# Performance work log

Measured on AMD Instinct MI355X. Metric: run time of the kernel, lower is better.

Reference implementation:

```python
import jax, jax.numpy as jnp
import numpy as np

EPS = 1e-8  # matches F.cosine_similarity default eps


def setup_inputs() -> dict:
    key = jax.random.key(0)
    k1, k2 = jax.random.split(key)
    labels = jax.random.uniform(k1, (8192, 2), dtype=jnp.float32)  # argmax -> random 0/1
    datas = jax.random.normal(k2, (8192, 4096), dtype=jnp.float32)
    return {"labels": labels, "datas": datas}


def reference(labels, datas):
    # labels: [B, C] one-hot (C=2); datas: [B, D]
    lab = jnp.argmax(labels, axis=1)
    mask0 = (lab == 0).astype(datas.dtype)  # normal vectors
    mask1 = (lab == 1).astype(datas.dtype)  # except vectors
    n0 = jnp.sum(mask0)
    n1 = jnp.sum(mask1)

    # mean of label-0 rows (fixed-shape masked mean instead of boolean gather)
    mean_vec = jnp.sum(datas * mask0[:, None], axis=0) / jnp.maximum(n0, 1.0)  # [D]

    # batched cosine similarity of every row vs mean_vec (replaces per-row loop)
    x_norm = jnp.maximum(jnp.linalg.norm(datas, axis=1), EPS)  # [B]
    m_norm = jnp.maximum(jnp.linalg.norm(mean_vec), EPS)       # scalar
    cos = (datas @ mean_vec) / (x_norm * m_norm)               # [B]
    abs_cos = jnp.abs(cos)

    sim_loss = jnp.sum(mask0 * (1.0 - abs_cos)) / jnp.maximum(n0, 1.0)
    differ_loss = jnp.sum(mask1 * abs_cos) / jnp.maximum(n1, 1.0)

    # edge cases: no normals -> both 0; normals but no excepts -> differ 0
    sim_loss = jnp.where(n0 > 0, sim_loss, 0.0)
    differ_loss = jnp.where((n0 > 0) & (n1 > 0), differ_loss, 0.0)
    total_loss = sim_loss + differ_loss
    return (total_loss, sim_loss, differ_loss)
```

## Files before the change

kernel.cpp:

```cpp
#include <hip/hip_runtime.h>
#include <math.h>

#define NROWS 8192
#define NCOLS 4096
#define NC4 1024
#define EPS 1e-8f

__device__ float g_partials[256 * NCOLS];
__device__ float g_S[NCOLS];
__device__ float g_n0[256];
__device__ float g_msq[64];
__device__ float g_A[2048];
__device__ float g_B[2048];

__global__ __launch_bounds__(1024) void k_colsum(const float* __restrict__ labels,
                                                 const float* __restrict__ datas) {
    const int b = blockIdx.x, t = threadIdx.x;
    const int r0 = b * 32;
    __shared__ float shm[32];
    if (t < 32) {
        float l0 = labels[2 * (r0 + t)];
        float l1 = labels[2 * (r0 + t) + 1];
        shm[t] = (l0 >= l1) ? 1.f : 0.f;
    }
    __syncthreads();
    if (t == 0) {
        float c = 0.f;
        #pragma unroll
        for (int r = 0; r < 32; ++r) c += shm[r];
        g_n0[b] = c;
    }
    const float4* d4 = (const float4*)datas;
    float4 acc = {0.f, 0.f, 0.f, 0.f};
    for (int r = 0; r < 32; ++r) {
        if (shm[r] != 0.f) {
            float4 v = d4[(size_t)(r0 + r) * NC4 + t];
            acc.x += v.x; acc.y += v.y; acc.z += v.z; acc.w += v.w;
        }
    }
    ((float4*)g_partials)[(size_t)b * NC4 + t] = acc;
}

__global__ __launch_bounds__(1024) void k_reduceS() {
    const int t = threadIdx.x, b = blockIdx.x;
    const int col = t & 63, sub = t >> 6;
    const int c = b * 64 + col;
    float s = 0.f;
    #pragma unroll
    for (int j = 0; j < 16; ++j)
        s += g_partials[(size_t)(sub * 16 + j) * NCOLS + c];
    __shared__ float sh[16][65];
    sh[sub][col] = s;
    __syncthreads();
    if (t < 64) {
        float tot = 0.f;
        #pragma unroll
        for (int i = 0; i < 16; ++i) tot += sh[i][t];
        g_S[c] = tot;
        float sq = tot * tot;
        #pragma unroll
        for (int off = 32; off; off >>= 1) sq += __shfl_xor(sq, off);
        if (t == 0) g_msq[b] = sq;
    }
}

__global__ __launch_bounds__(256) void k_cos(const float* __restrict__ labels,
                                             const float* __restrict__ datas) {
    const int t = threadIdx.x, lane = t & 63, w = t >> 6;
    const int r = blockIdx.x * 4 + w;
    const float4* d4 = (const float4*)datas;
    const float4* s4 = (const float4*)g_S;
    const size_t base = (size_t)r * NC4;
    float dot = 0.f, sq = 0.f;
    float4 v[8];
    #pragma unroll
    for (int half = 0; half < 2; ++half) {
        #pragma unroll
        for (int k = 0; k < 8; ++k)
            v[k] = d4[base + lane + ((half * 8 + k) << 6)];
        #pragma unroll
        for (int k = 0; k < 8; ++k) {
            float4 sv = s4[lane + ((half * 8 + k) << 6)];
            dot += v[k].x * sv.x + v[k].y * sv.y + v[k].z * sv.z + v[k].w * sv.w;
            sq  += v[k].x * v[k].x + v[k].y * v[k].y + v[k].z * v[k].z + v[k].w * v[k].w;
        }
    }
    #pragma unroll
    for (int off = 32; off; off >>= 1) {
        dot += __shfl_xor(dot, off);
        sq  += __shfl_xor(sq, off);
    }
    __shared__ float shA[4], shB[4];
    if (lane == 0) {
        float a = fabsf(dot) / fmaxf(sqrtf(sq), EPS);
        float l0 = labels[2 * r], l1 = labels[2 * r + 1];
        bool m0 = (l0 >= l1);
        shA[w] = m0 ? a : 0.f;
        shB[w] = m0 ? 0.f : a;
    }
    __syncthreads();
    if (t == 0) {
        g_A[blockIdx.x] = shA[0] + shA[1] + shA[2] + shA[3];
        g_B[blockIdx.x] = shB[0] + shB[1] + shB[2] + shB[3];
    }
}

__global__ __launch_bounds__(1024) void k_final(float* __restrict__ out) {
    const int t = threadIdx.x, lane = t & 63, w = t >> 6;
    float A = g_A[t] + g_A[t + 1024];
    float B = g_B[t] + g_B[t + 1024];
    float n0 = (t < 256) ? g_n0[t] : 0.f;
    float msq = (t < 64) ? g_msq[t] : 0.f;
    #pragma unroll
    for (int off = 32; off; off >>= 1) {
        A   += __shfl_xor(A, off);
        B   += __shfl_xor(B, off);
        n0  += __shfl_xor(n0, off);
        msq += __shfl_xor(msq, off);
    }
    __shared__ float sh[16][4];
    if (lane == 0) { sh[w][0] = A; sh[w][1] = B; sh[w][2] = n0; sh[w][3] = msq; }
    __syncthreads();
    if (t == 0) {
        float At = 0.f, Bt = 0.f, n0t = 0.f, mt = 0.f;
        #pragma unroll
        for (int i = 0; i < 16; ++i) {
            At += sh[i][0]; Bt += sh[i][1]; n0t += sh[i][2]; mt += sh[i][3];
        }
        float n1 = (float)NROWS - n0t;
        float n0d = fmaxf(n0t, 1.f), n1d = fmaxf(n1, 1.f);
        float D = fmaxf(sqrtf(mt), n0d * EPS);
        float simL = (n0t > 0.f) ? (n0t - At / D) / n0d : 0.f;
        float difL = (n0t > 0.f && n1 > 0.f) ? (Bt / D) / n1d : 0.f;
        out[0] = simL + difL;
        out[1] = simL;
        out[2] = difL;
    }
}

extern "C" void kernel_launch(void* const* d_in, const int* in_sizes, int n_in,
                              void* d_out, int out_size, void* d_ws, size_t ws_size,
                              hipStream_t stream) {
    const float* labels = (const float*)d_in[0];
    const float* datas  = (const float*)d_in[1];
    float* out = (float*)d_out;

    k_colsum<<<256, 1024, 0, stream>>>(labels, datas);
    k_reduceS<<<64, 1024, 0, stream>>>();
    k_cos<<<2048, 256, 0, stream>>>(labels, datas);
    k_final<<<1, 1024, 0, stream>>>(out);
}
```

Measured before the change: 208.7 us.

## Compact masked rows, split colsum blocks, stage mean in LDS, fuse final reduction

The column-sum kernel now builds a compacted list of label-0 row indices, splits each 32-row group across four 256-thread blocks, and unrolls the loads four ways so more memory requests are in flight. The cosine kernel stages the mean vector in shared memory, and the per-block partials are combined with global atomics. A last-block-done counter then computes the final losses in place, which removes the separate final kernel launch. In exchange it adds atomic contention on two scalars, float atomics that make the result order-dependent, and a per-block LDS preload.

Measured after the change: 300.6 us. 44.1% more time.

```diff
diff --git a/kernel.cpp b/kernel.cpp
--- a/kernel.cpp
+++ b/kernel.cpp
@@ -10,39 +10,60 @@
 __device__ float g_S[NCOLS];
 __device__ float g_n0[256];
 __device__ float g_msq[64];
-__device__ float g_A[2048];
-__device__ float g_B[2048];
+__device__ float g_Aacc, g_Bacc;
+__device__ int   g_cnt;
 
-__global__ __launch_bounds__(1024) void k_colsum(const float* __restrict__ labels,
-                                                 const float* __restrict__ datas) {
+__global__ __launch_bounds__(256) void k_colsum(const float* __restrict__ labels,
+                                                const float* __restrict__ datas) {
     const int b = blockIdx.x, t = threadIdx.x;
-    const int r0 = b * 32;
-    __shared__ float shm[32];
+    const int rg = b >> 2, q = b & 3;
+    const int r0 = rg * 32;
+    __shared__ float m[32];
+    __shared__ int idx[32];
+    __shared__ int cntS;
     if (t < 32) {
         float l0 = labels[2 * (r0 + t)];
         float l1 = labels[2 * (r0 + t) + 1];
-        shm[t] = (l0 >= l1) ? 1.f : 0.f;
+        m[t] = (l0 >= l1) ? 1.f : 0.f;
     }
     __syncthreads();
     if (t == 0) {
-        float c = 0.f;
+        int c = 0;
         #pragma unroll
-        for (int r = 0; r < 32; ++r) c += shm[r];
-        g_n0[b] = c;
+        for (int r = 0; r < 32; ++r) if (m[r] != 0.f) idx[c++] = r0 + r;
+        cntS = c;
+        if (q == 0) g_n0[rg] = (float)c;
     }
+    __syncthreads();
+    const int cnt = cntS;
+    const int coff = q * 256 + t;
     const float4* d4 = (const float4*)datas;
-    float4 acc = {0.f, 0.f, 0.f, 0.f};
-    for (int r = 0; r < 32; ++r) {
-        if (shm[r] != 0.f) {
-            float4 v = d4[(size_t)(r0 + r) * NC4 + t];
-            acc.x += v.x; acc.y += v.y; acc.z += v.z; acc.w += v.w;
-        }
+    float4 a0 = {0,0,0,0}, a1 = {0,0,0,0}, a2 = {0,0,0,0}, a3 = {0,0,0,0};
+    int j = 0;
+    for (; j + 3 < cnt; j += 4) {
+        float4 v0 = d4[(size_t)idx[j]     * NC4 + coff];
+        float4 v1 = d4[(size_t)idx[j + 1] * NC4 + coff];
+        float4 v2 = d4[(size_t)idx[j + 2] * NC4 + coff];
+        float4 v3 = d4[(size_t)idx[j + 3] * NC4 + coff];
+        a0.x += v0.x; a0.y += v0.y; a0.z += v0.z; a0.w += v0.w;
+        a1.x += v1.x; a1.y += v1.y; a1.z += v1.z; a1.w += v1.w;
+        a2.x += v2.x; a2.y += v2.y; a2.z += v2.z; a2.w += v2.w;
+        a3.x += v3.x; a3.y += v3.y; a3.z += v3.z; a3.w += v3.w;
     }
-    ((float4*)g_partials)[(size_t)b * NC4 + t] = acc;
+    for (; j < cnt; ++j) {
+        float4 v = d4[(size_t)idx[j] * NC4 + coff];
+        a0.x += v.x; a0.y += v.y; a0.z += v.z; a0.w += v.w;
+    }
+    a0.x += a1.x + a2.x + a3.x;
+    a0.y += a1.y + a2.y + a3.y;
+    a0.z += a1.z + a2.z + a3.z;
+    a0.w += a1.w + a2.w + a3.w;
+    ((float4*)g_partials)[(size_t)rg * NC4 + coff] = a0;
 }
 
 __global__ __launch_bounds__(1024) void k_reduceS() {
     const int t = threadIdx.x, b = blockIdx.x;
+    if (b == 0 && t == 0) { g_Aacc = 0.f; g_Bacc = 0.f; g_cnt = 0; }
     const int col = t & 63, sub = t >> 6;
     const int c = b * 64 + col;
     float s = 0.f;
@@ -65,11 +86,17 @@
 }
 
 __global__ __launch_bounds__(256) void k_cos(const float* __restrict__ labels,
-                                             const float* __restrict__ datas) {
+                                             const float* __restrict__ datas,
+                                             float* __restrict__ out) {
     const int t = threadIdx.x, lane = t & 63, w = t >> 6;
     const int r = blockIdx.x * 4 + w;
+    __shared__ float4 sS[NC4];
+    const float4* s4g = (const float4*)g_S;
+    #pragma unroll
+    for (int k = 0; k < 4; ++k) sS[t + k * 256] = s4g[t + k * 256];
+    __syncthreads();
+
     const float4* d4 = (const float4*)datas;
-    const float4* s4 = (const float4*)g_S;
     const size_t base = (size_t)r * NC4;
     float dot = 0.f, sq = 0.f;
     float4 v[8];
@@ -80,7 +107,7 @@
             v[k] = d4[base + lane + ((half * 8 + k) << 6)];
         #pragma unroll
         for (int k = 0; k < 8; ++k) {
-            float4 sv = s4[lane + ((half * 8 + k) << 6)];
+            float4 sv = sS[lane + ((half * 8 + k) << 6)];
             dot += v[k].x * sv.x + v[k].y * sv.y + v[k].z * sv.z + v[k].w * sv.w;
             sq  += v[k].x * v[k].x + v[k].y * v[k].y + v[k].z * v[k].z + v[k].w * v[k].w;
         }
@@ -91,6 +118,7 @@
         sq  += __shfl_xor(sq, off);
     }
     __shared__ float shA[4], shB[4];
+    __shared__ int shLast;
     if (lane == 0) {
         float a = fabsf(dot) / fmaxf(sqrtf(sq), EPS);
         float l0 = labels[2 * r], l1 = labels[2 * r + 1];
@@ -100,41 +128,40 @@
     }
     __syncthreads();
     if (t == 0) {
-        g_A[blockIdx.x] = shA[0] + shA[1] + shA[2] + shA[3];
-        g_B[blockIdx.x] = shB[0] + shB[1] + shB[2] + shB[3];
+        atomicAdd(&g_Aacc, shA[0] + shA[1] + shA[2] + shA[3]);
+        atomicAdd(&g_Bacc, shB[0] + shB[1] + shB[2] + shB[3]);
+        __threadfence();
+        int old = atomicAdd(&g_cnt, 1);
+        shLast = (old == gridDim.x - 1) ? 1 : 0;
     }
-}
-
-__global__ __launch_bounds__(1024) void k_final(float* __restrict__ out) {
-    const int t = threadIdx.x, lane = t & 63, w = t >> 6;
-    float A = g_A[t] + g_A[t + 1024];
-    float B = g_B[t] + g_B[t + 1024];
-    float n0 = (t < 256) ? g_n0[t] : 0.f;
-    float msq = (t < 64) ? g_msq[t] : 0.f;
-    #pragma unroll
-    for (int off = 32; off; off >>= 1) {
-        A   += __shfl_xor(A, off);
-        B   += __shfl_xor(B, off);
-        n0  += __shfl_xor(n0, off);
-        msq += __shfl_xor(msq, off);
-    }
-    __shared__ float sh[16][4];
-    if (lane == 0) { sh[w][0] = A; sh[w][1] = B; sh[w][2] = n0; sh[w][3] = msq; }
     __syncthreads();
-    if (t == 0) {
-        float At = 0.f, Bt = 0.f, n0t = 0.f, mt = 0.f;
+    if (shLast) {
+        __threadfence();
+        float n0 = g_n0[t & 255];
+        float msq = (t < 64) ? g_msq[t] : 0.f;
+        if (t >= 256) n0 = 0.f;
         #pragma unroll
-        for (int i = 0; i < 16; ++i) {
-            At += sh[i][0]; Bt += sh[i][1]; n0t += sh[i][2]; mt += sh[i][3];
+        for (int off = 32; off; off >>= 1) {
+            n0  += __shfl_xor(n0, off);
+            msq += __shfl_xor(msq, off);
         }
-        float n1 = (float)NROWS - n0t;
-        float n0d = fmaxf(n0t, 1.f), n1d = fmaxf(n1, 1.f);
-        float D = fmaxf(sqrtf(mt), n0d * EPS);
-        float simL = (n0t > 0.f) ? (n0t - At / D) / n0d : 0.f;
-        float difL = (n0t > 0.f && n1 > 0.f) ? (Bt / D) / n1d : 0.f;
-        out[0] = simL + difL;
-        out[1] = simL;
-        out[2] = difL;
+        __shared__ float shn[4], shm2[4];
+        if (lane == 0) { shn[w] = n0; shm2[w] = msq; }
+        __syncthreads();
+        if (t == 0) {
+            float n0t = shn[0] + shn[1] + shn[2] + shn[3];
+            float mt  = shm2[0] + shm2[1] + shm2[2] + shm2[3];
+            float At = atomicAdd(&g_Aacc, 0.f);
+            float Bt = atomicAdd(&g_Bacc, 0.f);
+            float n1 = (float)NROWS - n0t;
+            float n0d = fmaxf(n0t, 1.f), n1d = fmaxf(n1, 1.f);
+            float D = fmaxf(sqrtf(mt), n0d * EPS);
+            float simL = (n0t > 0.f) ? (n0t - At / D) / n0d : 0.f;
+            float difL = (n0t > 0.f && n1 > 0.f) ? (Bt / D) / n1d : 0.f;
+            out[0] = simL + difL;
+            out[1] = simL;
+            out[2] = difL;
+        }
     }
 }
 
@@ -145,8 +172,7 @@
     const float* datas  = (const float*)d_in[1];
     float* out = (float*)d_out;
 
-    k_colsum<<<256, 1024, 0, stream>>>(labels, datas);
+    k_colsum<<<1024, 256, 0, stream>>>(labels, datas);
     k_reduceS<<<64, 1024, 0, stream>>>();
-    k_cos<<<2048, 256, 0, stream>>>(labels, datas);
-    k_final<<<1, 1024, 0, stream>>>(out);
+    k_cos<<<2048, 256, 0, stream>>>(labels, datas, out);
 }
```
